# Kernel tuning notes

Measured on AMD Instinct MI355X. Metric: run time of the kernel, lower is better.

The kernel has to match this reference:

```python
import jax, jax.numpy as jnp
import numpy as np

B, VIN, C_IN = 8, 4096, 64
VOUT, E, S, C_OUT = 16384, 49152, 9, 32


def setup_inputs() -> dict:
    key = jax.random.key(0)
    ks = jax.random.split(key, 10)
    x = jax.random.normal(ks[0], (B, VIN, C_IN), dtype=jnp.float32)
    trans_row = jax.random.randint(ks[1], (E,), 0, VOUT)  # unused in math (matches original)
    trans_col = jax.random.randint(ks[2], (E,), 0, VIN)
    trans_value = jax.random.uniform(ks[3], (E,), dtype=jnp.float32)
    row_map = jax.random.randint(ks[4], (VOUT, 3), 0, E)
    indices = jax.random.randint(ks[5], (VOUT, S), 0, VOUT)  # spiral neighbor indices
    Wd = jax.random.normal(ks[6], (C_IN, S), dtype=jnp.float32) * 0.1  # depthwise kernel
    bd = jax.random.normal(ks[7], (C_IN,), dtype=jnp.float32) * 0.1
    Wp = jax.random.normal(ks[8], (C_OUT, C_IN), dtype=jnp.float32) * 0.1  # pointwise linear
    bp = jax.random.normal(ks[9], (C_OUT,), dtype=jnp.float32) * 0.1
    return {"x": x, "trans_row": trans_row, "trans_col": trans_col,
            "trans_value": trans_value, "row_map": row_map, "indices": indices,
            "Wd": Wd, "bd": bd, "Wp": Wp, "bp": bp}


def reference(x, trans_row, trans_col, trans_value, row_map, indices, Wd, bd, Wp, bp):
    # --- Pool: COO gather-scale + 3-way gather-and-sum ---
    edge = x[:, trans_col, :] * trans_value[None, :, None]          # [B, E, C]
    pooled = (edge[:, row_map[:, 0], :]
              + edge[:, row_map[:, 1], :]
              + edge[:, row_map[:, 2], :])                          # [B, Vout, C]
    # --- DSConv: spiral gather -> depthwise reduce over spiral -> pointwise ---
    sp = pooled[:, indices, :]                                      # [B, Vout, S, C]
    dw = jnp.einsum('bvsc,cs->bvc', sp, Wd) + bd                    # depthwise Conv2d(C,C,[1,S],groups=C)
    pw = jnp.einsum('bvc,oc->bvo', dw, Wp) + bp                     # pointwise Linear
    return jax.nn.relu(pw)                                          # [B, Vout, C_out]
```

## Files before the change

### kernel.cpp

```cpp
#include <hip/hip_runtime.h>

#define BATCH   8
#define VIN     4096
#define CIN     64
#define VOUTN   16384
#define SN      9
#define COUT    32
#define VT      64
#define UPB     16

__device__ __forceinline__ unsigned short f2bf(float f) {
  unsigned u = __float_as_uint(f);
  u += 0x7FFFu + ((u >> 16) & 1u);
  return (unsigned short)(u >> 16);
}
__device__ __forceinline__ float bf2f(unsigned short h) {
  return __uint_as_float((unsigned)h << 16);
}

__global__ __launch_bounds__(256) void pool_kernel(
    const float* __restrict__ x, const int* __restrict__ trans_col,
    const float* __restrict__ trans_value, const int* __restrict__ row_map,
    unsigned short* __restrict__ pooled) {
  __shared__ int   scol[UPB * 3];
  __shared__ float sval[UPB * 3];
  int t  = threadIdx.x;
  int b  = blockIdx.x & 7;
  int u0 = (blockIdx.x >> 3) * UPB;
  if (t < UPB * 3) {
    int e   = row_map[u0 * 3 + t];
    scol[t] = trans_col[e];
    sval[t] = trans_value[e];
  }
  __syncthreads();
  int g = t >> 4, l = t & 15;
  const float4* xb4 = (const float4*)(x + (size_t)b * VIN * CIN);
  float4 acc = make_float4(0.f, 0.f, 0.f, 0.f);
#pragma unroll
  for (int j = 0; j < 3; ++j) {
    int   col = scol[g * 3 + j];
    float tv  = sval[g * 3 + j];
    float4 p  = xb4[col * 16 + l];
    acc.x += tv * p.x; acc.y += tv * p.y; acc.z += tv * p.z; acc.w += tv * p.w;
  }
  ushort4 h;
  h.x = f2bf(acc.x); h.y = f2bf(acc.y); h.z = f2bf(acc.z); h.w = f2bf(acc.w);
  ((ushort4*)(pooled + (size_t)((b << 14) + u0 + g) * CIN))[l] = h;
}

__global__ __launch_bounds__(256) void dwpw_kernel(
    const unsigned short* __restrict__ pooled, const int* __restrict__ indices,
    const float* __restrict__ Wd, const float* __restrict__ bd,
    const float* __restrict__ Wp, const float* __restrict__ bp,
    float* __restrict__ out) {
  __shared__ float dw[VT][65];
  __shared__ int   sidx[VT * SN];
  __shared__ float swdT[SN * CIN];
  int t  = threadIdx.x;
  int b  = blockIdx.x & 7;
  int v0 = (blockIdx.x >> 3) * VT;

  for (int i = t; i < VT * SN; i += 256) {
    sidx[i] = indices[v0 * SN + i];
    int c = i / SN, s = i - c * SN;
    swdT[s * CIN + c] = Wd[i];
  }
  __syncthreads();

  int g = t >> 4, l = t & 15, c4 = l * 4;
  float4 wd4[SN];
#pragma unroll
  for (int s = 0; s < SN; ++s) wd4[s] = *(const float4*)&swdT[s * CIN + c4];
  float4 bd4 = *(const float4*)(bd + c4);
  const ushort4* pb4 = (const ushort4*)(pooled + (size_t)(b << 14) * CIN);

#pragma unroll
  for (int vi = 0; vi < 4; ++vi) {
    int vl = g + vi * 16;
    float4 acc = bd4;
#pragma unroll
    for (int s = 0; s < SN; ++s) {
      int u = sidx[vl * SN + s];
      ushort4 h = pb4[u * 16 + l];
      acc.x += wd4[s].x * bf2f(h.x);
      acc.y += wd4[s].y * bf2f(h.y);
      acc.z += wd4[s].z * bf2f(h.z);
      acc.w += wd4[s].w * bf2f(h.w);
    }
    dw[vl][c4 + 0] = acc.x; dw[vl][c4 + 1] = acc.y;
    dw[vl][c4 + 2] = acc.z; dw[vl][c4 + 3] = acc.w;
  }
  __syncthreads();

  int vl = t & 63;
  int w  = t >> 6;
  int ob = __builtin_amdgcn_readfirstlane(w * 8);
  float acc[8];
#pragma unroll
  for (int oo = 0; oo < 8; ++oo) acc[oo] = bp[ob + oo];
#pragma unroll 8
  for (int cc = 0; cc < CIN; ++cc) {
    float d = dw[vl][cc];
#pragma unroll
    for (int oo = 0; oo < 8; ++oo)
      acc[oo] += d * Wp[(ob + oo) * CIN + cc];
  }
  float* op = out + (size_t)((b << 14) + v0 + vl) * COUT + ob;
  float4 r0 = make_float4(fmaxf(acc[0], 0.f), fmaxf(acc[1], 0.f),
                          fmaxf(acc[2], 0.f), fmaxf(acc[3], 0.f));
  float4 r1 = make_float4(fmaxf(acc[4], 0.f), fmaxf(acc[5], 0.f),
                          fmaxf(acc[6], 0.f), fmaxf(acc[7], 0.f));
  *(float4*)op = r0;
  *(float4*)(op + 4) = r1;
}

extern "C" void kernel_launch(void* const* d_in, const int* in_sizes, int n_in,
                              void* d_out, int out_size, void* d_ws, size_t ws_size,
                              hipStream_t stream) {
  const float* x    = (const float*)d_in[0];
  const int*   tc   = (const int*)d_in[2];
  const float* tv   = (const float*)d_in[3];
  const int*   rm   = (const int*)d_in[4];
  const int*   idx  = (const int*)d_in[5];
  const float* Wd   = (const float*)d_in[6];
  const float* bd   = (const float*)d_in[7];
  const float* Wp   = (const float*)d_in[8];
  const float* bp   = (const float*)d_in[9];
  float* out = (float*)d_out;
  unsigned short* pooled = (unsigned short*)d_ws;

  pool_kernel<<<BATCH * (VOUTN / UPB), 256, 0, stream>>>(x, tc, tv, rm, pooled);
  dwpw_kernel<<<BATCH * (VOUTN / VT), 256, 0, stream>>>(pooled, idx, Wd, bd, Wp, bp, out);
}
```

Before: 114.5 us.

## Enlarge pool tiles, load Wd directly, vectorize LDS access, use nontemporal stores

The pool kernel now handles 64 output vertices per block, looping four times, so there are fewer blocks and less per-block setup. The dwpw kernel drops the shared transposed Wd buffer and has each thread read its Wd slice straight from global memory. It also preloads the spiral indices into registers, stores and reads dw rows as float4 with stride 68, and writes output with nontemporal stores. Together these cut shared-memory traffic and launch overhead, at the cost of higher register pressure and uncoalesced per-thread Wd loads.

Result: slower. 121.1 us (+5.7%).

```diff
diff --git a/kernel.cpp b/kernel.cpp
--- a/kernel.cpp
+++ b/kernel.cpp
@@ -7,7 +7,9 @@
 #define SN      9
 #define COUT    32
 #define VT      64
-#define UPB     16
+#define UPB     64
+
+typedef float f32x4 __attribute__((ext_vector_type(4)));
 
 __device__ __forceinline__ unsigned short f2bf(float f) {
   unsigned u = __float_as_uint(f);
@@ -35,17 +37,22 @@
   __syncthreads();
   int g = t >> 4, l = t & 15;
   const float4* xb4 = (const float4*)(x + (size_t)b * VIN * CIN);
-  float4 acc = make_float4(0.f, 0.f, 0.f, 0.f);
+  unsigned short* pb = pooled + (size_t)((b << 14) + u0) * CIN;
 #pragma unroll
-  for (int j = 0; j < 3; ++j) {
-    int   col = scol[g * 3 + j];
-    float tv  = sval[g * 3 + j];
-    float4 p  = xb4[col * 16 + l];
-    acc.x += tv * p.x; acc.y += tv * p.y; acc.z += tv * p.z; acc.w += tv * p.w;
+  for (int k = 0; k < UPB / 16; ++k) {
+    int ug = g + k * 16;
+    float4 acc = make_float4(0.f, 0.f, 0.f, 0.f);
+#pragma unroll
+    for (int j = 0; j < 3; ++j) {
+      int   col = scol[ug * 3 + j];
+      float tv  = sval[ug * 3 + j];
+      float4 p  = xb4[col * 16 + l];
+      acc.x += tv * p.x; acc.y += tv * p.y; acc.z += tv * p.z; acc.w += tv * p.w;
+    }
+    ushort4 h;
+    h.x = f2bf(acc.x); h.y = f2bf(acc.y); h.z = f2bf(acc.z); h.w = f2bf(acc.w);
+    ((ushort4*)(pb + (size_t)ug * CIN))[l] = h;
   }
-  ushort4 h;
-  h.x = f2bf(acc.x); h.y = f2bf(acc.y); h.z = f2bf(acc.z); h.w = f2bf(acc.w);
-  ((ushort4*)(pooled + (size_t)((b << 14) + u0 + g) * CIN))[l] = h;
 }
 
 __global__ __launch_bounds__(256) void dwpw_kernel(
@@ -53,65 +60,72 @@
     const float* __restrict__ Wd, const float* __restrict__ bd,
     const float* __restrict__ Wp, const float* __restrict__ bp,
     float* __restrict__ out) {
-  __shared__ float dw[VT][65];
+  __shared__ float dw[VT][68];
   __shared__ int   sidx[VT * SN];
-  __shared__ float swdT[SN * CIN];
   int t  = threadIdx.x;
   int b  = blockIdx.x & 7;
   int v0 = (blockIdx.x >> 3) * VT;
 
-  for (int i = t; i < VT * SN; i += 256) {
+  for (int i = t; i < VT * SN; i += 256)
     sidx[i] = indices[v0 * SN + i];
-    int c = i / SN, s = i - c * SN;
-    swdT[s * CIN + c] = Wd[i];
-  }
-  __syncthreads();
 
   int g = t >> 4, l = t & 15, c4 = l * 4;
+  float wflat[36];
+#pragma unroll
+  for (int q = 0; q < 9; ++q)
+    *(float4*)&wflat[q * 4] = *(const float4*)&Wd[c4 * SN + q * 4];
   float4 wd4[SN];
 #pragma unroll
-  for (int s = 0; s < SN; ++s) wd4[s] = *(const float4*)&swdT[s * CIN + c4];
+  for (int s = 0; s < SN; ++s)
+    wd4[s] = make_float4(wflat[s], wflat[9 + s], wflat[18 + s], wflat[27 + s]);
   float4 bd4 = *(const float4*)(bd + c4);
   const ushort4* pb4 = (const ushort4*)(pooled + (size_t)(b << 14) * CIN);
+  __syncthreads();
 
 #pragma unroll
   for (int vi = 0; vi < 4; ++vi) {
     int vl = g + vi * 16;
+    int us[SN];
+#pragma unroll
+    for (int s = 0; s < SN; ++s) us[s] = sidx[vl * SN + s];
     float4 acc = bd4;
 #pragma unroll
     for (int s = 0; s < SN; ++s) {
-      int u = sidx[vl * SN + s];
-      ushort4 h = pb4[u * 16 + l];
+      ushort4 h = pb4[us[s] * 16 + l];
       acc.x += wd4[s].x * bf2f(h.x);
       acc.y += wd4[s].y * bf2f(h.y);
       acc.z += wd4[s].z * bf2f(h.z);
       acc.w += wd4[s].w * bf2f(h.w);
     }
-    dw[vl][c4 + 0] = acc.x; dw[vl][c4 + 1] = acc.y;
-    dw[vl][c4 + 2] = acc.z; dw[vl][c4 + 3] = acc.w;
+    *(float4*)&dw[vl][c4] = acc;
   }
   __syncthreads();
 
   int vl = t & 63;
   int w  = t >> 6;
   int ob = __builtin_amdgcn_readfirstlane(w * 8);
+  const float* wpo = Wp + ob * CIN;
   float acc[8];
 #pragma unroll
   for (int oo = 0; oo < 8; ++oo) acc[oo] = bp[ob + oo];
-#pragma unroll 8
-  for (int cc = 0; cc < CIN; ++cc) {
-    float d = dw[vl][cc];
 #pragma unroll
-    for (int oo = 0; oo < 8; ++oo)
-      acc[oo] += d * Wp[(ob + oo) * CIN + cc];
+  for (int q = 0; q < 16; ++q) {
+    float4 d4 = *(const float4*)&dw[vl][q * 4];
+#pragma unroll
+    for (int oo = 0; oo < 8; ++oo) {
+      acc[oo] += d4.x * wpo[oo * CIN + q * 4 + 0];
+      acc[oo] += d4.y * wpo[oo * CIN + q * 4 + 1];
+      acc[oo] += d4.z * wpo[oo * CIN + q * 4 + 2];
+      acc[oo] += d4.w * wpo[oo * CIN + q * 4 + 3];
+    }
   }
   float* op = out + (size_t)((b << 14) + v0 + vl) * COUT + ob;
-  float4 r0 = make_float4(fmaxf(acc[0], 0.f), fmaxf(acc[1], 0.f),
-                          fmaxf(acc[2], 0.f), fmaxf(acc[3], 0.f));
-  float4 r1 = make_float4(fmaxf(acc[4], 0.f), fmaxf(acc[5], 0.f),
-                          fmaxf(acc[6], 0.f), fmaxf(acc[7], 0.f));
-  *(float4*)op = r0;
-  *(float4*)(op + 4) = r1;
+  f32x4 r0 = { fmaxf(acc[0], 0.f), fmaxf(acc[1], 0.f),
+               fmaxf(acc[2], 0.f), fmaxf(acc[3], 0.f) };
+  f32x4 r1 = { fmaxf(acc[4], 0.f), fmaxf(acc[5], 0.f),
+               fmaxf(acc[6], 0.f), fmaxf(acc[7], 0.f) };
+  __builtin_nontemporal_store(r0, (f32x4*)op);
+  __builtin_nontemporal_store(r1, (f32x4*)(op + 4));
 }
 
 extern "C" void kernel_launch(void* const* d_in, const int* in_sizes, int n_in,
```
